# Optimization experiments

Hardware: AMD Instinct MI355X
Metric: run time of the kernel (lower is better)

The kernel has to match this reference:

```python
import jax, jax.numpy as jnp
import numpy as np

B, V, T, D, NC = 512, 4, 16, 512, 174
EPS = 1e-5
_edges = np.ones((V, V)) - np.eye(V)
SEND = np.where(_edges)[0]   # [12]
RECV = np.where(_edges)[1]   # [12]
E2N = jnp.asarray(np.eye(V)[RECV].T, dtype=jnp.float32)  # [V, E] one-hot recv matrix


def _bn(x, g, b):
    # BatchNorm1d in training mode: batch stats over flattened rows, biased var
    m = x.mean(axis=0)
    v = jnp.var(x, axis=0)
    return (x - m) * jax.lax.rsqrt(v + EPS) * g + b


def _mlp(x, w1, b1, w2, b2, g, bb):
    # RefNRIMLP: Linear-ELU-(Dropout p=0.1 disabled/eval)-Linear-ELU-BN
    h = jax.nn.elu(x @ w1 + b1)
    h = jax.nn.elu(h @ w2 + b2)
    return _bn(h, g, bb)


def setup_inputs() -> dict:
    key = jax.random.key(0)
    ks = iter(jax.random.split(key, 64))
    def W(*s):
        return jax.random.normal(next(ks), s, dtype=jnp.float32) * 0.02
    def zeros(*s):
        return jnp.zeros(s, jnp.float32)
    def ones(*s):
        return jnp.ones(s, jnp.float32)
    return dict(
        global_img_input=zeros(1),
        box_categories=jax.random.randint(next(ks), (B, T, V), 0, 3),
        box_input=jax.random.uniform(next(ks), (B, T, V, 4), dtype=jnp.float32),
        hand_id=jax.random.randint(next(ks), (B,), 0, 2),
        video_label=jax.random.randint(next(ks), (B,), 0, NC),
        emb=W(3, D // 2),
        c2f_w1=W(4, D // 2), c2f_g1=ones(D // 2), c2f_b1=zeros(D // 2),
        c2f_w2=W(D // 2, D), c2f_g2=ones(D), c2f_b2=zeros(D),
        fus_w=W(D + D // 2, D), fus_g=ones(D), fus_b=zeros(D),
        m1_w1=W(2 * D, D), m1_b1=zeros(D), m1_w2=W(D, D), m1_b2=zeros(D), m1_g=ones(D), m1_bb=zeros(D),
        m2_w1=W(D, D), m2_b1=zeros(D), m2_w2=W(D, D), m2_b2=zeros(D), m2_g=ones(D), m2_bb=zeros(D),
        t1_w1=W(2 * D, D), t1_b1=zeros(D), t1_w2=W(D, D), t1_b2=zeros(D), t1_g=ones(D), t1_bb=zeros(D),
        ps_w1=W(D, D), ps_g1=ones(D), ps_b1=zeros(D), ps_w2=W(D, D), ps_g2=ones(D), ps_b2=zeros(D),
        tb_w1=W(T * D, D), tb_g1=ones(D), tb_b1=zeros(D), tb_w2=W(D, D), tb_g2=ones(D), tb_b2=zeros(D),
        cl_w1=W(D, D), cl_b1=zeros(D), cl_w2=W(D, 512), cl_b2=zeros(512),
        cl_w3=W(512, NC), cl_b3=zeros(NC),
    )


def reference(global_img_input, box_categories, box_input, hand_id, video_label,
              emb, c2f_w1, c2f_g1, c2f_b1, c2f_w2, c2f_g2, c2f_b2,
              fus_w, fus_g, fus_b,
              m1_w1, m1_b1, m1_w2, m1_b2, m1_g, m1_bb,
              m2_w1, m2_b1, m2_w2, m2_b2, m2_g, m2_bb,
              t1_w1, t1_b1, t1_w2, t1_b2, t1_g, t1_bb,
              ps_w1, ps_g1, ps_b1, ps_w2, ps_g2, ps_b2,
              tb_w1, tb_g1, tb_b1, tb_w2, tb_g2, tb_b2,
              cl_w1, cl_b1, cl_w2, cl_b2, cl_w3, cl_b3):
    b = hand_id.shape[0]
    # [b,T,V,*] -> [b,V,T,*] -> flatten rows
    x = box_input.transpose(0, 2, 1, 3).reshape(-1, 4)          # [b*V*T, 4]
    cats = box_categories.transpose(0, 2, 1).reshape(-1)        # [b*V*T]
    pad_mask = (jnp.arange(3)[:, None] != 0).astype(emb.dtype)  # padding_idx=0
    ce = (emb * pad_mask)[cats]                                 # [b*V*T, D/2]
    # coord_to_feature: Linear(no bias)-BN-ReLU x2
    h = jax.nn.relu(_bn(x @ c2f_w1, c2f_g1, c2f_b1))
    h = jax.nn.relu(_bn(h @ c2f_w2, c2f_g2, c2f_b2))
    # coord_category_fusion
    bf = jax.nn.relu(_bn(jnp.concatenate([h, ce], axis=1) @ fus_w, fus_g, fus_b))
    bf = bf.reshape(b, V, T, D)
    # node2edge gather + mlp1
    e = jnp.concatenate([bf[:, SEND], bf[:, RECV]], axis=-1).reshape(-1, 2 * D)
    e = _mlp(e, m1_w1, m1_b1, m1_w2, m1_b2, m1_g, m1_bb).reshape(b, len(SEND), T, D)
    # edge2node: one-hot matmul aggregation / (V-1)
    n = jnp.einsum('ve,betd->bvtd', E2N, e) / (V - 1)
    n = _mlp(n.reshape(-1, D), m2_w1, m2_b1, m2_w2, m2_b2, m2_g, m2_bb).reshape(b, V, T, D)
    # temporal MLP on cat(node, bf)
    p = jnp.concatenate([n, bf], axis=-1).reshape(-1, 2 * D)
    p = _mlp(p, t1_w1, t1_b1, t1_w2, t1_b2, t1_g, t1_bb)
    # point_spatial_node_fusion
    p = jax.nn.relu(_bn(p @ ps_w1, ps_g1, ps_b1))
    p = jax.nn.relu(_bn(p @ ps_w2, ps_g2, ps_b2))
    # t_box_feature_fusion over flattened time
    q = p.reshape(b * V, T * D)
    q = jax.nn.relu(_bn(q @ tb_w1, tb_g1, tb_b1))
    q = jax.nn.relu(_bn(q @ tb_w2, tb_g2, tb_b2))
    feat = q.reshape(b, V, D).mean(axis=1)                      # mean over boxes
    h1 = jax.nn.relu(feat @ cl_w1 + cl_b1)
    h2 = jax.nn.relu(h1 @ cl_w2 + cl_b2)
    pf = h2 @ cl_w3 + cl_b3                                      # [b, NC]
    return (pf, video_label)
```

## Files before the change

kernel.cpp:

```cpp
#include <hip/hip_runtime.h>
#include <math.h>

#define EPS_ 1e-5f

static constexpr int Bb = 512, Vv = 4, Tt = 16, Dd = 512, NCc = 174;
static constexpr int NROW = Bb * Vv * Tt;
static constexpr int EROW = Bb * 12 * Tt;
static constexpr int CB = 128;
static constexpr int NCHUNK = Bb / CB;
static constexpr int CROWS_N = CB * Vv * Tt;
static constexpr int CROWS_E = CB * 12 * Tt;

__constant__ int d_SEND[12] = {0,0,0,1,1,1,2,2,2,3,3,3};
__constant__ int d_RECV[12] = {1,2,3,0,2,3,0,1,3,0,1,2};
__constant__ int d_EOFV[4][3] = {{3,6,9},{0,7,10},{1,4,11},{2,5,8}};

typedef float f32x4 __attribute__((ext_vector_type(4)));
typedef short s16x8 __attribute__((ext_vector_type(8)));

static __device__ __forceinline__ float b2f(unsigned short u) {
    union { unsigned int i; float f; } x; x.i = ((unsigned int)u) << 16; return x.f;
}
static __device__ __forceinline__ unsigned short f2b(float f) {
    union { float f; unsigned int i; } x; x.f = f;
    unsigned int r = (x.i + 0x7fffu + ((x.i >> 16) & 1u)) >> 16;
    return (unsigned short)r;
}
static __device__ __forceinline__ float act_f(float v, int act) {
    if (act == 1) return fmaxf(v, 0.f);
    if (act == 2) return (v > 0.f) ? v : (__expf(v) - 1.f);
    return v;
}

#define GL2LDS(g, l) __builtin_amdgcn_global_load_lds(                     \
    (__attribute__((address_space(1))) void*)(g),                          \
    (__attribute__((address_space(3))) void*)(l), 16, 0, 0)

#define CS_STRIDE 136

__global__ __launch_bounds__(256) void gemm_bf16(
    const unsigned short* __restrict__ A0, int Ka0, int K0,
    const unsigned short* __restrict__ A1, int Ka1, int K1,
    const unsigned short* __restrict__ WT, int Kw, int wtoff,
    unsigned short* __restrict__ C, int M, int N,
    const float* __restrict__ bias, int act,
    float* __restrict__ pstats, int accum,
    float* __restrict__ Cpart, int Ksl)
{
    __shared__ __align__(16) unsigned short SMEM[24576];
    int tid = threadIdx.x;
    int lane = tid & 63, wave = tid >> 6;
    int wr = wave >> 1, wc = wave & 1;
    int g = lane >> 4, r16 = lane & 15;

    int nct = N >> 7, nrt = M >> 7;
    int id = blockIdx.x, bx, by;
    if ((nrt & 7) == 0) {
        int grp = id / (nct * 8);
        int rem = id - grp * nct * 8;
        by = grp * 8 + (rem & 7);
        bx = rem >> 3;
    } else { bx = id % nct; by = id / nct; }
    int rowBase = by * 128;
    int colBase = bx * 128;
    int koff = blockIdx.z * Ksl;

    int srow = wave * 32 + (lane >> 2);
    int scol = (lane & 3) * 8;
    const unsigned short* wrow  = WT + (size_t)(colBase + srow) * Kw + wtoff + scol;
    const unsigned short* wrow2 = WT + (size_t)(colBase + srow + 16) * Kw + wtoff + scol;

    f32x4 acc[4][4];
#pragma unroll
    for (int i = 0; i < 4; ++i)
#pragma unroll
        for (int j = 0; j < 4; ++j) acc[i][j] = (f32x4){0.f, 0.f, 0.f, 0.f};

#define STAGE_(kg_, SL_) do {                                                   \
        int kg = (kg_);                                                         \
        const unsigned short* Ap; int lda; int kc;                              \
        if (kg < K0) { Ap = A0; lda = Ka0; kc = kg; }                           \
        else         { Ap = A1; lda = Ka1; kc = kg - K0; }                      \
        const unsigned short* ga = Ap + (size_t)(rowBase + srow) * lda + kc + scol; \
        GL2LDS(ga, (SL_) + wave * 1024);                                        \
        GL2LDS(ga + (size_t)16 * lda, (SL_) + wave * 1024 + 512);               \
        GL2LDS(wrow + kg, (SL_) + 4096 + wave * 1024);                          \
        GL2LDS(wrow2 + kg, (SL_) + 4096 + wave * 1024 + 512);                   \
    } while (0)

    int nt = Ksl >> 5;
    STAGE_(koff, SMEM);
    if (nt > 1) STAGE_(koff + 32, SMEM + 8192);
    int cur = 0;
    for (int t = 0; t < nt; ++t) {
        if (t + 1 < nt) asm volatile("s_waitcnt vmcnt(4)" ::: "memory");
        else            asm volatile("s_waitcnt vmcnt(0)" ::: "memory");
        __builtin_amdgcn_s_barrier();
        __builtin_amdgcn_sched_barrier(0);
        if (t + 2 < nt) {
            int nx = cur + 2; if (nx >= 3) nx -= 3;
            STAGE_(koff + (t + 2) * 32, SMEM + nx * 8192);
        }
        unsigned short* SA = SMEM + cur * 8192;
        unsigned short* SB = SA + 4096;
        s16x8 xf[4], wf[4];
#pragma unroll
        for (int j = 0; j < 4; ++j)
            xf[j] = *(const s16x8*)(SA + (wr * 64 + j * 16 + r16) * 32 + g * 8);
#pragma unroll
        for (int i = 0; i < 4; ++i)
            wf[i] = *(const s16x8*)(SB + (wc * 64 + i * 16 + r16) * 32 + g * 8);
#pragma unroll
        for (int i = 0; i < 4; ++i)
#pragma unroll
            for (int j = 0; j < 4; ++j)
                acc[i][j] = __builtin_amdgcn_mfma_f32_16x16x32_bf16(
                    wf[i], xf[j], acc[i][j], 0, 0, 0);
        cur = (cur == 2) ? 0 : cur + 1;
    }
#undef STAGE_
    __syncthreads();

    if (Cpart) {
#pragma unroll
        for (int j = 0; j < 4; ++j) {
            int row = rowBase + wr * 64 + j * 16 + r16;
#pragma unroll
            for (int i = 0; i < 4; ++i) {
                int col0 = colBase + wc * 64 + i * 16 + g * 4;
                float4 v = make_float4(acc[i][j][0], acc[i][j][1],
                                       acc[i][j][2], acc[i][j][3]);
                *(float4*)&Cpart[((size_t)blockIdx.z * M + row) * N + col0] = v;
            }
        }
        return;
    }

#pragma unroll
    for (int i = 0; i < 4; ++i) {
        int lc0 = wc * 64 + i * 16 + g * 4;
        float4 b4 = bias ? *(const float4*)(bias + colBase + lc0)
                         : make_float4(0.f, 0.f, 0.f, 0.f);
        float s[4] = {0.f, 0.f, 0.f, 0.f}, q[4] = {0.f, 0.f, 0.f, 0.f};
#pragma unroll
        for (int j = 0; j < 4; ++j) {
            int lr = wr * 64 + j * 16 + r16;
            float v0 = act_f(acc[i][j][0] + b4.x, act);
            float v1 = act_f(acc[i][j][1] + b4.y, act);
            float v2 = act_f(acc[i][j][2] + b4.z, act);
            float v3 = act_f(acc[i][j][3] + b4.w, act);
            *(ushort4*)&SMEM[lr * CS_STRIDE + lc0] =
                make_ushort4(f2b(v0), f2b(v1), f2b(v2), f2b(v3));
            s[0] += v0; s[1] += v1; s[2] += v2; s[3] += v3;
            q[0] += v0 * v0; q[1] += v1 * v1; q[2] += v2 * v2; q[3] += v3 * v3;
        }
        if (pstats) {
#pragma unroll
            for (int p = 0; p < 4; ++p) {
#pragma unroll
                for (int d = 1; d < 16; d <<= 1) {
                    s[p] += __shfl_xor(s[p], d);
                    q[p] += __shfl_xor(q[p], d);
                }
            }
            if (r16 == 0) {
                float* pr = pstats + ((size_t)(by * 2 + wr)) * 1024 + colBase + lc0;
                float4 s4 = make_float4(s[0], s[1], s[2], s[3]);
                float4 q4 = make_float4(q[0], q[1], q[2], q[3]);
                if (accum) {
                    float4 o = *(float4*)pr;
                    s4.x += o.x; s4.y += o.y; s4.z += o.z; s4.w += o.w;
                    float4 o2 = *(float4*)(pr + 512);
                    q4.x += o2.x; q4.y += o2.y; q4.z += o2.z; q4.w += o2.w;
                }
                *(float4*)pr = s4;
                *(float4*)(pr + 512) = q4;
            }
        }
    }
    __syncthreads();
    {
        int qd = tid & 3;
        int rr = tid >> 2;
#pragma unroll
        for (int pass = 0; pass < 2; ++pass) {
            int lr = pass * 64 + rr;
            size_t grow = (size_t)(rowBase + lr) * N + colBase;
#pragma unroll
            for (int u = 0; u < 4; ++u) {
                int cofs = u * 32 + qd * 8;
                uint4 v = *(const uint4*)(SMEM + lr * CS_STRIDE + cofs);
                *(uint4*)&C[grow + cofs] = v;
            }
        }
    }
}

__global__ __launch_bounds__(256) void finalize_stats_k(
    const float* __restrict__ P, int nrows, float* __restrict__ slot)
{
    __shared__ float red[256];
    int lane = threadIdx.x & 63;
    int seg  = threadIdx.x >> 6;
    int col  = blockIdx.x * 64 + lane;
    float s = 0.f;
    for (int r = seg; r < nrows; r += 4)
        s += P[(size_t)r * 1024 + col];
    red[threadIdx.x] = s;
    __syncthreads();
    if (seg == 0)
        slot[col] = red[lane] + red[64 + lane] + red[128 + lane] + red[192 + lane];
}

__global__ __launch_bounds__(256) void combine_k(
    const float4* __restrict__ P, int S, int M,
    unsigned short* __restrict__ C, float* __restrict__ pstats, int act)
{
    int col4 = threadIdx.x & 127;
    int rh = threadIdx.x >> 7;
    int rb = blockIdx.y * 8;
    float4 s4 = make_float4(0.f, 0.f, 0.f, 0.f);
    float4 q4 = make_float4(0.f, 0.f, 0.f, 0.f);
#pragma unroll
    for (int i = 0; i < 4; ++i) {
        int row = rb + rh + 2 * i;
        float4 v = make_float4(0.f, 0.f, 0.f, 0.f);
#pragma unroll
        for (int z = 0; z < 8; ++z) {
            float4 p = P[((size_t)z * M + row) * 128 + col4];
            v.x += p.x; v.y += p.y; v.z += p.z; v.w += p.w;
        }
        v.x = act_f(v.x, act); v.y = act_f(v.y, act);
        v.z = act_f(v.z, act); v.w = act_f(v.w, act);
        ((ushort4*)C)[(size_t)row * 128 + col4] =
            make_ushort4(f2b(v.x), f2b(v.y), f2b(v.z), f2b(v.w));
        s4.x += v.x; s4.y += v.y; s4.z += v.z; s4.w += v.w;
        q4.x += v.x * v.x; q4.y += v.y * v.y; q4.z += v.z * v.z; q4.w += v.w * v.w;
    }
    __shared__ float4 sb[256], qb[256];
    sb[threadIdx.x] = s4; qb[threadIdx.x] = q4;
    __syncthreads();
    if (threadIdx.x < 128) {
        float4 a = sb[threadIdx.x], b = sb[threadIdx.x + 128];
        float4 c = qb[threadIdx.x], d = qb[threadIdx.x + 128];
        int col = threadIdx.x * 4;
        float* pr = pstats + (size_t)blockIdx.y * 1024 + col;
        *(float4*)pr = make_float4(a.x + b.x, a.y + b.y, a.z + b.z, a.w + b.w);
        *(float4*)(pr + 512) = make_float4(c.x + d.x, c.y + d.y, c.z + d.z, c.w + d.w);
    }
}

#define NTD 13
struct TBatch {
    const float* src[NTD];
    unsigned short* dst[NTD];
    int K[NTD];
    int tbase[NTD + 1];
};
__global__ __launch_bounds__(256) void transpose_batch_k(TBatch tb)
{
    int id = blockIdx.x;
    int d = 0;
#pragma unroll
    for (int j = 0; j < NTD; ++j) if (id >= tb.tbase[j + 1]) d = j + 1;
    int rel = id - tb.tbase[d];
    int kt = rel >> 3, ntl = rel & 7;
    int k0 = kt * 64, n0 = ntl * 64;
    const float* S = tb.src[d];
    unsigned short* D = tb.dst[d];
    int K = tb.K[d];
    __shared__ unsigned short L[64][68];
    int c = threadIdx.x & 63;
    int r = threadIdx.x >> 6;
#pragma unroll
    for (int p = 0; p < 16; ++p) {
        int kk = r + p * 4;
        L[kk][c] = f2b(S[(size_t)(k0 + kk) * 512 + n0 + c]);
    }
    __syncthreads();
#pragma unroll
    for (int p = 0; p < 16; ++p) {
        int nn = r + p * 4;
        D[(size_t)(n0 + nn) * K + k0 + c] = L[c][nn];
    }
}

__global__ __launch_bounds__(256) void transpose_pq_k(
    const float* __restrict__ W, unsigned short* __restrict__ WT)
{
    int id = blockIdx.x;
    int kt = id >> 4, ntl = id & 15;
    int k0 = kt * 64, n0 = ntl * 64;
    __shared__ unsigned short L[64][68];
    int c = threadIdx.x & 63;
    int r = threadIdx.x >> 6;
    int nb = n0 + c;
    const float* S = (n0 < 512) ? (W + nb) : (W + (size_t)512 * 512 + (nb - 512));
#pragma unroll
    for (int p = 0; p < 16; ++p) {
        int kk = r + p * 4;
        L[kk][c] = f2b(S[(size_t)(k0 + kk) * 512]);
    }
    __syncthreads();
#pragma unroll
    for (int p = 0; p < 16; ++p) {
        int nn = r + p * 4;
        WT[(size_t)(n0 + nn) * 512 + k0 + c] = L[c][nn];
    }
}

__global__ __launch_bounds__(256) void colstats_k(
    const unsigned short* __restrict__ X, float* __restrict__ P)
{
    __shared__ float sb[256][4], qb[256][4];
    int c4 = threadIdx.x & 63;
    int seg = threadIdx.x >> 6;
    int r0 = blockIdx.x * 128;
    float s[4] = {0.f, 0.f, 0.f, 0.f}, q[4] = {0.f, 0.f, 0.f, 0.f};
    for (int r = r0 + seg; r < r0 + 128; r += 4) {
        ushort4 x = ((const ushort4*)X)[(size_t)r * 64 + c4];
        float v0 = b2f(x.x), v1 = b2f(x.y), v2 = b2f(x.z), v3 = b2f(x.w);
        s[0] += v0; s[1] += v1; s[2] += v2; s[3] += v3;
        q[0] += v0 * v0; q[1] += v1 * v1; q[2] += v2 * v2; q[3] += v3 * v3;
    }
#pragma unroll
    for (int e = 0; e < 4; ++e) { sb[threadIdx.x][e] = s[e]; qb[threadIdx.x][e] = q[e]; }
    __syncthreads();
    if (threadIdx.x < 64) {
        int c = threadIdx.x;
        float4 S, Q;
        S.x = sb[c][0] + sb[c + 64][0] + sb[c + 128][0] + sb[c + 192][0];
        S.y = sb[c][1] + sb[c + 64][1] + sb[c + 128][1] + sb[c + 192][1];
        S.z = sb[c][2] + sb[c + 64][2] + sb[c + 128][2] + sb[c + 192][2];
        S.w = sb[c][3] + sb[c + 64][3] + sb[c + 128][3] + sb[c + 192][3];
        Q.x = qb[c][0] + qb[c + 64][0] + qb[c + 128][0] + qb[c + 192][0];
        Q.y = qb[c][1] + qb[c + 64][1] + qb[c + 128][1] + qb[c + 192][1];
        Q.z = qb[c][2] + qb[c + 64][2] + qb[c + 128][2] + qb[c + 192][2];
        Q.w = qb[c][3] + qb[c + 64][3] + qb[c + 128][3] + qb[c + 192][3];
        *(float4*)&P[(size_t)blockIdx.x * 1024 + c * 4] = S;
        *(float4*)&P[(size_t)blockIdx.x * 1024 + 512 + c * 4] = Q;
    }
}

__global__ __launch_bounds__(256) void bn_apply_k(
    unsigned short* __restrict__ X, long n4, int cmask4, int C,
    const float* __restrict__ slot, const float* __restrict__ gm,
    const float* __restrict__ bt, float inv_cnt, float premul, int act)
{
    __shared__ float sc_s[512], sh_s[512];
    for (int c = threadIdx.x; c < C; c += 256) {
        float mean = slot[c] * inv_cnt;
        float var = fmaxf(slot[512 + c] * inv_cnt - mean * mean, 0.f);
        float sc = gm[c] * rsqrtf(var + EPS_);
        sc_s[c] = sc * premul;
        sh_s[c] = bt[c] - mean * sc;
    }
    __syncthreads();
    long stride = (long)gridDim.x * 256;
    for (long i = (long)blockIdx.x * 256 + threadIdx.x; i < n4; i += stride) {
        ushort4 x = ((ushort4*)X)[i];
        int c = ((int)(i & cmask4)) * 4;
        unsigned short o[4] = {x.x, x.y, x.z, x.w};
#pragma unroll
        for (int e = 0; e < 4; ++e) {
            float v = b2f(o[e]) * sc_s[c + e] + sh_s[c + e];
            o[e] = f2b(act_f(v, act));
        }
        ((ushort4*)X)[i] = make_ushort4(o[0], o[1], o[2], o[3]);
    }
}

__global__ __launch_bounds__(256) void zero_k(float* p, int n)
{
    int i = blockIdx.x * 256 + threadIdx.x;
    if (i < n) p[i] = 0.f;
}

__global__ __launch_bounds__(256) void build_x0_k(
    const float* __restrict__ box, float* __restrict__ X0)
{
    int i = blockIdx.x * 256 + threadIdx.x;
    if (i >= NROW * 4) return;
    int c = i & 3; int r = i >> 2;
    int t = r & 15; int bv = r >> 4; int v = bv & 3; int b = bv >> 2;
    X0[i] = box[(((size_t)b * Tt + t) * Vv + v) * 4 + c];
}

__global__ __launch_bounds__(256) void build_ce_k(
    const int* __restrict__ cats, const float* __restrict__ emb,
    unsigned short* __restrict__ CE)
{
    int i = blockIdx.x * 256 + threadIdx.x;
    if (i >= NROW * 64) return;
    int c4 = i & 63; int r = i >> 6;
    int t = r & 15; int bv = r >> 4; int v = bv & 3; int b = bv >> 2;
    int cat = cats[((size_t)b * Tt + t) * Vv + v];
    unsigned short o[4];
#pragma unroll
    for (int e = 0; e < 4; ++e)
        o[e] = (cat == 0) ? 0 : f2b(emb[cat * 256 + c4 * 4 + e]);
    ((ushort4*)CE)[(size_t)r * 64 + c4] = make_ushort4(o[0], o[1], o[2], o[3]);
}

__global__ __launch_bounds__(256) void smallk_gemm_k(
    const float* __restrict__ X0, const float* __restrict__ W4,
    unsigned short* __restrict__ Y1)
{
    int i = blockIdx.x * 256 + threadIdx.x;
    if (i >= NROW * 64) return;
    int n4 = i & 63; int m = i >> 6;
    float4 x = *(const float4*)(X0 + m * 4);
    unsigned short o[4];
#pragma unroll
    for (int e = 0; e < 4; ++e) {
        int n = n4 * 4 + e;
        float v = x.x * W4[n] + x.y * W4[256 + n] + x.z * W4[512 + n] + x.w * W4[768 + n];
        o[e] = f2b(v);
    }
    ((ushort4*)Y1)[(size_t)m * 64 + n4] = make_ushort4(o[0], o[1], o[2], o[3]);
}

__global__ __launch_bounds__(256) void edge_gather_k(
    const unsigned short* __restrict__ PQ,
    const float* __restrict__ b1, unsigned short* __restrict__ E)
{
    int i = blockIdx.x * 256 + threadIdx.x;
    if (i >= CROWS_E * 128) return;
    int c4 = i & 127; int m = i >> 7;
    int t = m & 15; int be = m >> 4; int e = be % 12; int brel = be / 12;
    int s = d_SEND[e], r = d_RECV[e];
    ushort4 p = ((const ushort4*)PQ)[(((size_t)brel * 4 + s) * 16 + t) * 256 + c4];
    ushort4 q = ((const ushort4*)PQ)[(((size_t)brel * 4 + r) * 16 + t) * 256 + 128 + c4];
    unsigned short pa[4] = {p.x, p.y, p.z, p.w}, qa[4] = {q.x, q.y, q.z, q.w}, o[4];
#pragma unroll
    for (int e2 = 0; e2 < 4; ++e2) {
        float v = b2f(pa[e2]) + b2f(qa[e2]) + b1[c4 * 4 + e2];
        o[e2] = f2b(act_f(v, 2));
    }
    ((ushort4*)E)[i] = make_ushort4(o[0], o[1], o[2], o[3]);
}

__global__ __launch_bounds__(256) void edge_agg_k(
    const unsigned short* __restrict__ E2c, unsigned short* __restrict__ nraw, int b0)
{
    int i = blockIdx.x * 256 + threadIdx.x;
    if (i >= CB * Vv * Tt * 128) return;
    int c4 = i & 127; int r = i >> 7;
    int t = r & 15; int r2 = r >> 4; int v = r2 & 3; int brel = r2 >> 2;
    float s[4] = {0.f, 0.f, 0.f, 0.f};
#pragma unroll
    for (int j = 0; j < 3; ++j) {
        int e = d_EOFV[v][j];
        ushort4 x = ((const ushort4*)E2c)[(((size_t)brel * 12 + e) * 16 + t) * 128 + c4];
        s[0] += b2f(x.x); s[1] += b2f(x.y); s[2] += b2f(x.z); s[3] += b2f(x.w);
    }
    ((ushort4*)nraw)[((((size_t)(b0 + brel)) * 4 + v) * 16 + t) * 128 + c4] =
        make_ushort4(f2b(s[0]), f2b(s[1]), f2b(s[2]), f2b(s[3]));
}

__global__ __launch_bounds__(256) void feat_mean_k(
    const unsigned short* __restrict__ q, unsigned short* __restrict__ feat)
{
    int i = blockIdx.x * 256 + threadIdx.x;
    if (i >= Bb * 128) return;
    int c4 = i & 127; int b = i >> 7;
    float s[4] = {0.f, 0.f, 0.f, 0.f};
#pragma unroll
    for (int v = 0; v < 4; ++v) {
        ushort4 x = ((const ushort4*)q)[(((size_t)b * 4 + v)) * 128 + c4];
        s[0] += b2f(x.x); s[1] += b2f(x.y); s[2] += b2f(x.z); s[3] += b2f(x.w);
    }
    ((ushort4*)feat)[(size_t)b * 128 + c4] = make_ushort4(
        f2b(0.25f * s[0]), f2b(0.25f * s[1]), f2b(0.25f * s[2]), f2b(0.25f * s[3]));
}

__global__ __launch_bounds__(256) void final_gemm_k(
    const unsigned short* __restrict__ H2, const float* __restrict__ W,
    const float* __restrict__ b, float* __restrict__ out)
{
    int i = blockIdx.x * 256 + threadIdx.x;
    if (i >= Bb * NCc) return;
    int n = i % NCc; int m = i / NCc;
    float s = b[n];
    for (int k = 0; k < 512; ++k)
        s += b2f(H2[(size_t)m * 512 + k]) * W[(size_t)k * NCc + n];
    out[i] = s;
}

__global__ __launch_bounds__(256) void copy_labels_k(
    const int* __restrict__ lab, float* __restrict__ out)
{
    int i = blockIdx.x * 256 + threadIdx.x;
    if (i < Bb) out[i] = (float)lab[i];
}

static inline void gemm(hipStream_t s,
                        const unsigned short* A0, int Ka0, int K0,
                        const unsigned short* A1, int Ka1, int K1,
                        const unsigned short* WT, int Kw, int wtoff,
                        unsigned short* C, int M, int N,
                        const float* bias, int act, float* pstats, int accum)
{
    dim3 g((N / 128) * (M / 128), 1, 1);
    hipLaunchKernelGGL(gemm_bf16, g, dim3(256), 0, s,
                       A0, Ka0, K0, A1, Ka1, K1, WT, Kw, wtoff, C, M, N,
                       bias, act, pstats, accum, (float*)nullptr, K0 + K1);
}

static inline void finalize(hipStream_t s, const float* P, int nrows, float* slot)
{
    hipLaunchKernelGGL(finalize_stats_k, dim3(16), dim3(256), 0, s, P, nrows, slot);
}

static inline void bn_apply(hipStream_t s, unsigned short* X, long n, int C,
                            const float* slot, const float* gm, const float* bt,
                            float cnt, float premul, int act)
{
    long n4 = n / 4;
    long nb = (n4 + 255) / 256;
    if (nb > 1024) nb = 1024;
    hipLaunchKernelGGL(bn_apply_k, dim3((unsigned)nb), dim3(256), 0, s,
                       X, n4, C / 4 - 1, C, slot, gm, bt, 1.f / cnt, premul, act);
}

extern "C" void kernel_launch(void* const* d_in, const int* in_sizes, int n_in,
                              void* d_out, int out_size, void* d_ws, size_t ws_size,
                              hipStream_t stream)
{
    const int*   box_cat = (const int*)  d_in[1];
    const float* box_in  = (const float*)d_in[2];
    const int*   vlabel  = (const int*)  d_in[4];
    const float* emb     = (const float*)d_in[5];
    const float* c2f_w1  = (const float*)d_in[6];
    const float* c2f_g1  = (const float*)d_in[7];
    const float* c2f_b1  = (const float*)d_in[8];
    const float* c2f_w2  = (const float*)d_in[9];
    const float* c2f_g2  = (const float*)d_in[10];
    const float* c2f_b2  = (const float*)d_in[11];
    const float* fus_w   = (const float*)d_in[12];
    const float* fus_g   = (const float*)d_in[13];
    const float* fus_b   = (const float*)d_in[14];
    const float* m1_w1   = (const float*)d_in[15];
    const float* m1_b1   = (const float*)d_in[16];
    const float* m1_w2   = (const float*)d_in[17];
    const float* m1_b2   = (const float*)d_in[18];
    const float* m1_g    = (const float*)d_in[19];
    const float* m1_bb   = (const float*)d_in[20];
    const float* m2_w1   = (const float*)d_in[21];
    const float* m2_b1   = (const float*)d_in[22];
    const float* m2_w2   = (const float*)d_in[23];
    const float* m2_b2   = (const float*)d_in[24];
    const float* m2_g    = (const float*)d_in[25];
    const float* m2_bb   = (const float*)d_in[26];
    const float* t1_w1   = (const float*)d_in[27];
    const float* t1_b1   = (const float*)d_in[28];
    const float* t1_w2   = (const float*)d_in[29];
    const float* t1_b2   = (const float*)d_in[30];
    const float* t1_g    = (const float*)d_in[31];
    const float* t1_bb   = (const float*)d_in[32];
    const float* ps_w1   = (const float*)d_in[33];
    const float* ps_g1   = (const float*)d_in[34];
    const float* ps_b1   = (const float*)d_in[35];
    const float* ps_w2   = (const float*)d_in[36];
    const float* ps_g2   = (const float*)d_in[37];
    const float* ps_b2   = (const float*)d_in[38];
    const float* tb_w1   = (const float*)d_in[39];
    const float* tb_g1   = (const float*)d_in[40];
    const float* tb_b1   = (const float*)d_in[41];
    const float* tb_w2   = (const float*)d_in[42];
    const float* tb_g2   = (const float*)d_in[43];
    const float* tb_b2   = (const float*)d_in[44];
    const float* cl_w1   = (const float*)d_in[45];
    const float* cl_b1   = (const float*)d_in[46];
    const float* cl_w2   = (const float*)d_in[47];
    const float* cl_b2   = (const float*)d_in[48];
    const float* cl_w3   = (const float*)d_in[49];
    const float* cl_b3   = (const float*)d_in[50];

    float* out = (float*)d_out;

    char* base = (char*)d_ws;
    const size_t SZ_ACT = (size_t)NROW * 512 * 2;
    unsigned short* A0v = (unsigned short*)(base);
    unsigned short* A1v = (unsigned short*)(base + SZ_ACT);
    char* Sreg = base + 2 * SZ_ACT;
    unsigned short* A2v = (unsigned short*)Sreg;
    unsigned short* CE  = (unsigned short*)Sreg;
    unsigned short* Y1  = (unsigned short*)(Sreg + (size_t)NROW * 256 * 2);
    unsigned short* PQc = (unsigned short*)Sreg;
    unsigned short* EC1 = (unsigned short*)(Sreg + (size_t)CROWS_N * 1024 * 2);
    unsigned short* EC2 = (unsigned short*)(Sreg + (size_t)CROWS_N * 1024 * 2
                                                 + (size_t)CROWS_E * 512 * 2);
    float* Ppart = (float*)Sreg;
    char* wtb = Sreg + (size_t)CROWS_N * 1024 * 2 + 2 * (size_t)CROWS_E * 512 * 2;
    unsigned short* wtp = (unsigned short*)wtb;
    size_t wo = 0;
    auto alloc_wt = [&](int K) { unsigned short* p = wtp + wo; wo += (size_t)K * 512; return p; };
    unsigned short* WTc2f2 = alloc_wt(256);
    unsigned short* WTfus  = alloc_wt(768);
    unsigned short* WTpq   = alloc_wt(1024);
    unsigned short* WTm1b  = alloc_wt(512);
    unsigned short* WTm2a  = alloc_wt(512);
    unsigned short* WTm2b  = alloc_wt(512);
    unsigned short* WTt1a  = alloc_wt(1024);
    unsigned short* WTt1b  = alloc_wt(512);
    unsigned short* WTps1  = alloc_wt(512);
    unsigned short* WTps2  = alloc_wt(512);
    unsigned short* WTtb1  = alloc_wt(8192);
    unsigned short* WTtb2  = alloc_wt(512);
    unsigned short* WTcl1  = alloc_wt(512);
    unsigned short* WTcl2  = alloc_wt(512);
    float* X0f    = (float*)(wtp + wo);
    float* STATS  = X0f + (size_t)NROW * 4;
    float* PSTATS = STATS + 10 * 1024;

    auto slot = [&](int i) { return STATS + (size_t)i * 1024; };

    {
        int nz = 10 * 1024 + 384 * 1024;
        hipLaunchKernelGGL(zero_k, dim3((nz + 255) / 256), dim3(256), 0, stream,
                           STATS, nz);
    }
    {
        TBatch tb;
        const float* srcs[NTD] = {c2f_w2, fus_w, m1_w2, m2_w1, m2_w2, t1_w1, t1_w2,
                                  ps_w1, ps_w2, tb_w1, tb_w2, cl_w1, cl_w2};
        unsigned short* dsts[NTD] = {WTc2f2, WTfus, WTm1b, WTm2a, WTm2b, WTt1a, WTt1b,
                                     WTps1, WTps2, WTtb1, WTtb2, WTcl1, WTcl2};
        int Ks[NTD] = {256, 768, 512, 512, 512, 1024, 512, 512, 512, 8192, 512, 512, 512};
        int acc = 0;
        for (int i = 0; i < NTD; ++i) {
            tb.src[i] = srcs[i]; tb.dst[i] = dsts[i]; tb.K[i] = Ks[i];
            tb.tbase[i] = acc; acc += (Ks[i] / 64) * 8;
        }
        tb.tbase[NTD] = acc;
        hipLaunchKernelGGL(transpose_batch_k, dim3((unsigned)acc), dim3(256), 0,
                           stream, tb);
    }
    hipLaunchKernelGGL(transpose_pq_k, dim3(128), dim3(256), 0, stream, m1_w1, WTpq);

    hipLaunchKernelGGL(build_x0_k, dim3((NROW * 4 + 255) / 256), dim3(256), 0, stream,
                       box_in, X0f);
    hipLaunchKernelGGL(build_ce_k, dim3((NROW * 64 + 255) / 256), dim3(256), 0, stream,
                       box_cat, emb, CE);

    hipLaunchKernelGGL(smallk_gemm_k, dim3((NROW * 64 + 255) / 256), dim3(256), 0,
                       stream, X0f, c2f_w1, Y1);
    hipLaunchKernelGGL(colstats_k, dim3(NROW / 128), dim3(256), 0, stream, Y1, PSTATS);
    finalize(stream, PSTATS, NROW / 128, slot(0));
    bn_apply(stream, Y1, (long)NROW * 256, 256, slot(0), c2f_g1, c2f_b1,
             (float)NROW, 1.f, 1);

    gemm(stream, Y1, 256, 256, nullptr, 0, 0, WTc2f2, 256, 0, A1v, NROW, 512,
         nullptr, 0, PSTATS, 0);
    finalize(stream, PSTATS, 512, slot(1));
    bn_apply(stream, A1v, (long)NROW * 512, 512, slot(1), c2f_g2, c2f_b2,
             (float)NROW, 1.f, 1);

    gemm(stream, A1v, 512, 512, CE, 256, 256, WTfus, 768, 0, A0v, NROW, 512,
         nullptr, 0, PSTATS, 0);
    finalize(stream, PSTATS, 512, slot(2));
    bn_apply(stream, A0v, (long)NROW * 512, 512, slot(2), fus_g, fus_b,
             (float)NROW, 1.f, 1);

    for (int c = 0; c < NCHUNK; ++c) {
        const unsigned short* BFc = A0v + (size_t)c * CROWS_N * 512;
        gemm(stream, BFc, 512, 512, nullptr, 0, 0, WTpq, 512, 0, PQc, CROWS_N, 1024,
             nullptr, 0, nullptr, 0);
        hipLaunchKernelGGL(edge_gather_k, dim3((CROWS_E * 128 + 255) / 256), dim3(256),
                           0, stream, PQc, m1_b1, EC1);
        gemm(stream, EC1, 512, 512, nullptr, 0, 0, WTm1b, 512, 0, EC2, CROWS_E, 512,
             m1_b2, 2, PSTATS, 1);
        hipLaunchKernelGGL(edge_agg_k, dim3((CB * Vv * Tt * 128 + 255) / 256), dim3(256),
                           0, stream, EC2, A1v, c * CB);
    }
    finalize(stream, PSTATS, 384, slot(3));
    bn_apply(stream, A1v, (long)NROW * 512, 512, slot(3), m1_g, m1_bb,
             (float)EROW, 1.f / 3.f, 0);

    gemm(stream, A1v, 512, 512, nullptr, 0, 0, WTm2a, 512, 0, A2v, NROW, 512,
         m2_b1, 2, nullptr, 0);
    gemm(stream, A2v, 512, 512, nullptr, 0, 0, WTm2b, 512, 0, A1v, NROW, 512,
         m2_b2, 2, PSTATS, 0);
    finalize(stream, PSTATS, 512, slot(4));
    bn_apply(stream, A1v, (long)NROW * 512, 512, slot(4), m2_g, m2_bb,
             (float)NROW, 1.f, 0);

    gemm(stream, A1v, 512, 512, A0v, 512, 512, WTt1a, 1024, 0, A2v, NROW, 512,
         t1_b1, 2, nullptr, 0);
    gemm(stream, A2v, 512, 512, nullptr, 0, 0, WTt1b, 512, 0, A1v, NROW, 512,
         t1_b2, 2, PSTATS, 0);
    finalize(stream, PSTATS, 512, slot(5));
    bn_apply(stream, A1v, (long)NROW * 512, 512, slot(5), t1_g, t1_bb,
             (float)NROW, 1.f, 0);

    gemm(stream, A1v, 512, 512, nullptr, 0, 0, WTps1, 512, 0, A2v, NROW, 512,
         nullptr, 0, PSTATS, 0);
    finalize(stream, PSTATS, 512, slot(6));
    bn_apply(stream, A2v, (long)NROW * 512, 512, slot(6), ps_g1, ps_b1,
             (float)NROW, 1.f, 1);

    gemm(stream, A2v, 512, 512, nullptr, 0, 0, WTps2, 512, 0, A0v, NROW, 512,
         nullptr, 0, PSTATS, 0);
    finalize(stream, PSTATS, 512, slot(7));
    bn_apply(stream, A0v, (long)NROW * 512, 512, slot(7), ps_g2, ps_b2,
             (float)NROW, 1.f, 1);

    {
        dim3 g((512 / 128) * (2048 / 128), 1, 8);
        hipLaunchKernelGGL(gemm_bf16, g, dim3(256), 0, stream,
                           A0v, 8192, 8192, (const unsigned short*)nullptr, 0, 0,
                           WTtb1, 8192, 0, A1v, 2048, 512,
                           (const float*)nullptr, 0, (float*)nullptr, 0, Ppart, 1024);
        hipLaunchKernelGGL(combine_k, dim3(1, 2048 / 8), dim3(256), 0, stream,
                           (const float4*)Ppart, 8, 2048, A1v, PSTATS, 0);
        finalize(stream, PSTATS, 2048 / 8, slot(8));
    }
    bn_apply(stream, A1v, (long)Bb * Vv * 512, 512, slot(8), tb_g1, tb_b1,
             (float)(Bb * Vv), 1.f, 1);

    gemm(stream, A1v, 512, 512, nullptr, 0, 0, WTtb2, 512, 0, A2v, Bb * Vv, 512,
         nullptr, 0, PSTATS, 0);
    finalize(stream, PSTATS, (Bb * Vv / 128) * 2, slot(9));
    bn_apply(stream, A2v, (long)Bb * Vv * 512, 512, slot(9), tb_g2, tb_b2,
             (float)(Bb * Vv), 1.f, 1);

    hipLaunchKernelGGL(feat_mean_k, dim3((Bb * 128 + 255) / 256), dim3(256), 0, stream,
                       A2v, A0v);

    gemm(stream, A0v, 512, 512, nullptr, 0, 0, WTcl1, 512, 0, A1v, Bb, 512,
         cl_b1, 1, nullptr, 0);
    gemm(stream, A1v, 512, 512, nullptr, 0, 0, WTcl2, 512, 0, A2v, Bb, 512,
         cl_b2, 1, nullptr, 0);
    hipLaunchKernelGGL(final_gemm_k, dim3((Bb * NCc + 255) / 256), dim3(256), 0, stream,
                       A2v, cl_w3, cl_b3, out);

    hipLaunchKernelGGL(copy_labels_k, dim3((Bb + 255) / 256), dim3(256), 0, stream,
                       vlabel, out + (size_t)Bb * NCc);
}
```

Baseline: 1.275 ms.

## Fold BatchNorm affine into next GEMM weights and bias; tile final classifier GEMM

Three of the BatchNorm apply passes that directly feed a linear layer are removed. Each BN scale is folded into the columns of the next layer's bf16 transposed weights, and its shift is folded into a new bias (shift times W plus the original bias) by a small kernel. This avoids reading and writing the full activation tensor three times, at the cost of rounding the scaled weights to bf16 again and running a serial 512-long loop per output to build each bias. Separately, the final 512x174 GEMM now stages 8 rows in shared memory per block and reuses each weight load across those rows.

New measurement: 1.399 ms. +9.7%, slower.

```diff
diff --git a/kernel.cpp b/kernel.cpp
--- a/kernel.cpp
+++ b/kernel.cpp
@@ -212,6 +212,36 @@
         slot[col] = red[lane] + red[64 + lane] + red[128 + lane] + red[192 + lane];
 }
 
+__global__ __launch_bounds__(256) void fold_bn_k(
+    const float* __restrict__ slot, const float* __restrict__ gm,
+    const float* __restrict__ bt, float inv_cnt, float premul,
+    unsigned short* __restrict__ WT, int Kw, int kof,
+    const float* __restrict__ Wsrc, const float* __restrict__ bias_in,
+    float* __restrict__ bias_out)
+{
+    int blk = blockIdx.x;
+    if (blk < 1024) {
+        int i = blk * 256 + threadIdx.x;
+        int n = i >> 9, k = i & 511;
+        float mean = slot[k] * inv_cnt;
+        float var = fmaxf(slot[512 + k] * inv_cnt - mean * mean, 0.f);
+        float sc = gm[k] * rsqrtf(var + EPS_) * premul;
+        unsigned short* p = &WT[(size_t)n * Kw + kof + k];
+        *p = f2b(b2f(*p) * sc);
+    } else {
+        int n = (blk - 1024) * 256 + threadIdx.x;
+        float acc = bias_in ? bias_in[n] : 0.f;
+        for (int k = 0; k < 512; ++k) {
+            float mean = slot[k] * inv_cnt;
+            float var = fmaxf(slot[512 + k] * inv_cnt - mean * mean, 0.f);
+            float sc = gm[k] * rsqrtf(var + EPS_);
+            float sh = bt[k] - mean * sc;
+            acc += sh * Wsrc[(size_t)k * 512 + n];
+        }
+        bias_out[n] = acc;
+    }
+}
+
 __global__ __launch_bounds__(256) void combine_k(
     const float4* __restrict__ P, int S, int M,
     unsigned short* __restrict__ C, float* __restrict__ pstats, int act)
@@ -478,13 +508,25 @@
     const unsigned short* __restrict__ H2, const float* __restrict__ W,
     const float* __restrict__ b, float* __restrict__ out)
 {
-    int i = blockIdx.x * 256 + threadIdx.x;
-    if (i >= Bb * NCc) return;
-    int n = i % NCc; int m = i / NCc;
-    float s = b[n];
-    for (int k = 0; k < 512; ++k)
-        s += b2f(H2[(size_t)m * 512 + k]) * W[(size_t)k * NCc + n];
-    out[i] = s;
+    __shared__ float Ls[8 * 512];
+    int m0 = blockIdx.x * 8;
+    for (int i = threadIdx.x; i < 1024; i += 256) {
+        ushort4 x = ((const ushort4*)H2)[(size_t)m0 * 128 + i];
+        *(float4*)&Ls[i * 4] = make_float4(b2f(x.x), b2f(x.y), b2f(x.z), b2f(x.w));
+    }
+    __syncthreads();
+    int n = threadIdx.x;
+    if (n >= NCc) return;
+    float acc[8];
+#pragma unroll
+    for (int m = 0; m < 8; ++m) acc[m] = b[n];
+    for (int k = 0; k < 512; ++k) {
+        float w = W[(size_t)k * NCc + n];
+#pragma unroll
+        for (int m = 0; m < 8; ++m) acc[m] += Ls[m * 512 + k] * w;
+    }
+#pragma unroll
+    for (int m = 0; m < 8; ++m) out[(size_t)(m0 + m) * NCc + n] = acc[m];
 }
 
 __global__ __launch_bounds__(256) void copy_labels_k(
@@ -521,6 +563,16 @@
     if (nb > 1024) nb = 1024;
     hipLaunchKernelGGL(bn_apply_k, dim3((unsigned)nb), dim3(256), 0, s,
                        X, n4, C / 4 - 1, C, slot, gm, bt, 1.f / cnt, premul, act);
+}
+
+static inline void fold_bn(hipStream_t s, const float* slot, const float* gm,
+                           const float* bt, float cnt, float premul,
+                           unsigned short* WT, int Kw, int kof,
+                           const float* Wsrc, const float* bias_in, float* bias_out)
+{
+    hipLaunchKernelGGL(fold_bn_k, dim3(1026), dim3(256), 0, s,
+                       slot, gm, bt, 1.f / cnt, premul, WT, Kw, kof,
+                       Wsrc, bias_in, bias_out);
 }
 
 extern "C" void kernel_launch(void* const* d_in, const int* in_sizes, int n_in,
@@ -613,6 +665,7 @@
     float* X0f    = (float*)(wtp + wo);
     float* STATS  = X0f + (size_t)NROW * 4;
     float* PSTATS = STATS + 10 * 1024;
+    float* BIASF  = PSTATS + 512 * 1024;
 
     auto slot = [&](int i) { return STATS + (size_t)i * 1024; };
 
@@ -675,27 +728,27 @@
                            0, stream, EC2, A1v, c * CB);
     }
     finalize(stream, PSTATS, 384, slot(3));
-    bn_apply(stream, A1v, (long)NROW * 512, 512, slot(3), m1_g, m1_bb,
-             (float)EROW, 1.f / 3.f, 0);
+    fold_bn(stream, slot(3), m1_g, m1_bb, (float)EROW, 1.f / 3.f,
+            WTm2a, 512, 0, m2_w1, m2_b1, BIASF);
 
     gemm(stream, A1v, 512, 512, nullptr, 0, 0, WTm2a, 512, 0, A2v, NROW, 512,
-         m2_b1, 2, nullptr, 0);
+         BIASF, 2, nullptr, 0);
     gemm(stream, A2v, 512, 512, nullptr, 0, 0, WTm2b, 512, 0, A1v, NROW, 512,
          m2_b2, 2, PSTATS, 0);
     finalize(stream, PSTATS, 512, slot(4));
-    bn_apply(stream, A1v, (long)NROW * 512, 512, slot(4), m2_g, m2_bb,
-             (float)NROW, 1.f, 0);
+    fold_bn(stream, slot(4), m2_g, m2_bb, (float)NROW, 1.f,
+            WTt1a, 1024, 0, t1_w1, t1_b1, BIASF + 512);
 
     gemm(stream, A1v, 512, 512, A0v, 512, 512, WTt1a, 1024, 0, A2v, NROW, 512,
-         t1_b1, 2, nullptr, 0);
+         BIASF + 512, 2, nullptr, 0);
     gemm(stream, A2v, 512, 512, nullptr, 0, 0, WTt1b, 512, 0, A1v, NROW, 512,
          t1_b2, 2, PSTATS, 0);
     finalize(stream, PSTATS, 512, slot(5));
-    bn_apply(stream, A1v, (long)NROW * 512, 512, slot(5), t1_g, t1_bb,
-             (float)NROW, 1.f, 0);
+    fold_bn(stream, slot(5), t1_g, t1_bb, (float)NROW, 1.f,
+            WTps1, 512, 0, ps_w1, nullptr, BIASF + 1024);
 
     gemm(stream, A1v, 512, 512, nullptr, 0, 0, WTps1, 512, 0, A2v, NROW, 512,
-         nullptr, 0, PSTATS, 0);
+         BIASF + 1024, 0, PSTATS, 0);
     finalize(stream, PSTATS, 512, slot(6));
     bn_apply(stream, A2v, (long)NROW * 512, 512, slot(6), ps_g1, ps_b1,
              (float)NROW, 1.f, 1);
@@ -732,7 +785,7 @@
          cl_b1, 1, nullptr, 0);
     gemm(stream, A1v, 512, 512, nullptr, 0, 0, WTcl2, 512, 0, A2v, Bb, 512,
          cl_b2, 1, nullptr, 0);
-    hipLaunchKernelGGL(final_gemm_k, dim3((Bb * NCc + 255) / 256), dim3(256), 0, stream,
+    hipLaunchKernelGGL(final_gemm_k, dim3(Bb / 8), dim3(256), 0, stream,
                        A2v, cl_w3, cl_b3, out);
 
     hipLaunchKernelGGL(copy_labels_k, dim3((Bb + 255) / 256), dim3(256), 0, stream,
```
